# Kernel optimization log

Measured on AMD Instinct MI355X. Metric: run time of the kernel, lower is better.

## Reference

```python
import jax, jax.numpy as jnp
import numpy as np

D_MODEL = 1024
N_HEADS = 16
HEAD_DIM = D_MODEL // N_HEADS


def setup_inputs() -> dict:
    key = jax.random.key(0)
    ks = jax.random.split(key, 7)
    scale = 1.0 / np.sqrt(D_MODEL)
    x = jax.random.normal(ks[0], (4, 2048, D_MODEL), dtype=jnp.float32)
    Wq = jax.random.normal(ks[1], (D_MODEL, D_MODEL), dtype=jnp.float32) * scale
    Wk = jax.random.normal(ks[2], (D_MODEL, D_MODEL), dtype=jnp.float32) * scale
    Wv = jax.random.normal(ks[3], (D_MODEL, D_MODEL), dtype=jnp.float32) * scale
    bq = jax.random.normal(ks[4], (D_MODEL,), dtype=jnp.float32) * scale
    bk = jax.random.normal(ks[5], (D_MODEL,), dtype=jnp.float32) * scale
    bv = jax.random.normal(ks[6], (D_MODEL,), dtype=jnp.float32) * scale
    return {"x": x, "Wq": Wq, "bq": bq, "Wk": Wk, "bk": bk, "Wv": Wv, "bv": bv}


def reference(x, Wq, bq, Wk, bk, Wv, bv):
    B, S, _ = x.shape
    # Linear projections (torch Linear: x @ W.T + b; W here stored as [in, out])
    q = x @ Wq + bq
    k = x @ Wk + bk
    v = x @ Wv + bv
    # [B, H, S, Dh]
    q = q.reshape(B, S, N_HEADS, HEAD_DIM).transpose(0, 2, 1, 3)
    k = k.reshape(B, S, N_HEADS, HEAD_DIM).transpose(0, 2, 1, 3)
    v = v.reshape(B, S, N_HEADS, HEAD_DIM).transpose(0, 2, 1, 3)
    scores = jnp.einsum("bhqd,bhkd->bhqk", q, k) / jnp.sqrt(jnp.float32(HEAD_DIM))
    probs = jax.nn.softmax(scores, axis=-1)
    out = jnp.einsum("bhqk,bhkd->bhqd", probs, v)
    return out.transpose(0, 2, 1, 3).reshape(B, S, D_MODEL)
```

## Files before the change

### kernel.cpp

```cpp
#include <hip/hip_runtime.h>
#include <math.h>

#define DM   1024
#define SEQ  2048
#define BAT  4
#define NH   16
#define DH   64
#define MTOT (BAT*SEQ)
#define NKT  (SEQ/64)

typedef __attribute__((ext_vector_type(8))) short bf16x8;
typedef __attribute__((ext_vector_type(4))) short bf16x4;
typedef __attribute__((ext_vector_type(4))) float f32x4;
typedef __attribute__((ext_vector_type(16))) float f32x16;
typedef __attribute__((ext_vector_type(4))) unsigned int u32x4;

static __device__ __forceinline__ unsigned short f2bf(float f) {
    union { float f; unsigned u; } x; x.f = f;
    unsigned r = x.u + 0x7fffu + ((x.u >> 16) & 1u);
    return (unsigned short)(r >> 16);
}

static __device__ __forceinline__ void load_lds16(const void* g, void* l) {
    __builtin_amdgcn_global_load_lds(
        (const __attribute__((address_space(1))) unsigned int*)g,
        (__attribute__((address_space(3))) unsigned int*)l,
        16, 0, 0);
}

__global__ __launch_bounds__(256)
void xcvt(const float* __restrict__ x, unsigned short* __restrict__ out, int n8)
{
    for (int i = blockIdx.x * blockDim.x + threadIdx.x; i < n8; i += gridDim.x * blockDim.x) {
        float4 a = reinterpret_cast<const float4*>(x)[2 * i];
        float4 b = reinterpret_cast<const float4*>(x)[2 * i + 1];
        ushort4 lo, hi;
        lo.x = f2bf(a.x); lo.y = f2bf(a.y); lo.z = f2bf(a.z); lo.w = f2bf(a.w);
        hi.x = f2bf(b.x); hi.y = f2bf(b.y); hi.z = f2bf(b.z); hi.w = f2bf(b.w);
        reinterpret_cast<ushort4*>(out)[2 * i]     = lo;
        reinterpret_cast<ushort4*>(out)[2 * i + 1] = hi;
    }
}

__global__ __launch_bounds__(256)
void wtcvt(const float* __restrict__ Wq, const float* __restrict__ Wk,
           const float* __restrict__ Wv, unsigned short* __restrict__ Wt)
{
    const float* W = (blockIdx.z == 0) ? Wq : (blockIdx.z == 1) ? Wk : Wv;
    unsigned short* out = Wt + (size_t)blockIdx.z * DM * DM;

    __shared__ float Ts[64][65];
    const int t  = threadIdx.x;
    const int k0 = blockIdx.y * 64;
    const int n0 = blockIdx.x * 64;

    const int r  = t >> 4;
    const int c4 = (t & 15) * 4;
#pragma unroll
    for (int u = 0; u < 4; ++u) {
        float4 v = *reinterpret_cast<const float4*>(&W[(size_t)(k0 + r + u * 16) * DM + n0 + c4]);
        Ts[r + u * 16][c4 + 0] = v.x;
        Ts[r + u * 16][c4 + 1] = v.y;
        Ts[r + u * 16][c4 + 2] = v.z;
        Ts[r + u * 16][c4 + 3] = v.w;
    }
    __syncthreads();

    const int n   = t >> 2;
    const int kk0 = (t & 3) * 16;
#pragma unroll
    for (int j = 0; j < 4; ++j) {
        ushort4 o;
        o.x = f2bf(Ts[kk0 + j * 4 + 0][n]);
        o.y = f2bf(Ts[kk0 + j * 4 + 1][n]);
        o.z = f2bf(Ts[kk0 + j * 4 + 2][n]);
        o.w = f2bf(Ts[kk0 + j * 4 + 3][n]);
        *reinterpret_cast<ushort4*>(&out[(size_t)(n0 + n) * DM + k0 + kk0 + j * 4]) = o;
    }
}

#define GBM 128
#define GBN 128
#define GBK 64
#define GNT (DM/GBK)

__global__ __launch_bounds__(256)
void qkv_mfma(const unsigned short* __restrict__ Xb,
              const unsigned short* __restrict__ Wt,
              const float* __restrict__ bq, const float* __restrict__ bk,
              const float* __restrict__ bv,
              unsigned short* __restrict__ Qw, unsigned short* __restrict__ Kw,
              unsigned short* __restrict__ Vt)
{
    __shared__ __align__(16) unsigned short As[2][GBM][GBK];
    __shared__ __align__(16) unsigned short Bs[2][GBN][GBK];

    const int t    = threadIdx.x;
    const int lane = t & 63;
    const int w    = t >> 6;
    const int g    = lane >> 4;
    const int c    = lane & 15;
    const int wm   = w >> 1;
    const int wn   = w & 1;

    const int cpx = gridDim.x >> 3;
    const int swz = (blockIdx.x & 7) * cpx + (blockIdx.x >> 3);
    const int tn  = swz % (3072 / GBN);
    const int tm  = swz / (3072 / GBN);
    const int m0  = tm * GBM;
    const int n0  = tn * GBN;

    const int srow  = lane >> 3;
    const int sswz  = ((lane & 7) * 16) ^ (16 * (srow & 7));
    const int rbase = w * 32;

#define GSTAGE(buf, kt)                                                               \
    do {                                                                              \
        const size_t kb = (size_t)(kt) * GBK;                                         \
        _Pragma("unroll")                                                             \
        for (int u = 0; u < 4; ++u) {                                                 \
            const int row = rbase + u * 8;                                            \
            load_lds16((const char*)(Xb + (size_t)(m0 + row + srow) * DM + kb) + sswz,\
                       (void*)&As[buf][row][0]);                                      \
        }                                                                             \
        _Pragma("unroll")                                                             \
        for (int u = 0; u < 4; ++u) {                                                 \
            const int row = rbase + u * 8;                                            \
            load_lds16((const char*)(Wt + (size_t)(n0 + row + srow) * DM + kb) + sswz,\
                       (void*)&Bs[buf][row][0]);                                      \
        }                                                                             \
    } while (0)

    f32x4 acc[4][4];
#pragma unroll
    for (int i = 0; i < 4; ++i)
#pragma unroll
        for (int j = 0; j < 4; ++j) { acc[i][j][0] = 0.f; acc[i][j][1] = 0.f; acc[i][j][2] = 0.f; acc[i][j][3] = 0.f; }

    GSTAGE(0, 0);

    for (int kt = 0; kt < GNT; ++kt) {
        const int cb = kt & 1;
        if (kt + 1 < GNT) GSTAGE(cb ^ 1, kt + 1);
        __syncthreads();

#pragma unroll
        for (int ks = 0; ks < 2; ++ks) {
            bf16x8 af[4], bf[4];
#pragma unroll
            for (int mb = 0; mb < 4; ++mb) {
                const int row = wm * 64 + mb * 16 + c;
                const int off = (ks * 64 + g * 16) ^ (16 * (row & 7));
                af[mb] = *reinterpret_cast<const bf16x8*>((const char*)&As[cb][row][0] + off);
            }
#pragma unroll
            for (int nb = 0; nb < 4; ++nb) {
                const int row = wn * 64 + nb * 16 + c;
                const int off = (ks * 64 + g * 16) ^ (16 * (row & 7));
                bf[nb] = *reinterpret_cast<const bf16x8*>((const char*)&Bs[cb][row][0] + off);
            }
#pragma unroll
            for (int mb = 0; mb < 4; ++mb)
#pragma unroll
                for (int nb = 0; nb < 4; ++nb)
                    acc[mb][nb] = __builtin_amdgcn_mfma_f32_16x16x32_bf16(af[mb], bf[nb], acc[mb][nb], 0, 0, 0);
        }

        __syncthreads();
    }

    const int p   = n0 >> 10;
    const int nl0 = (n0 & 1023) + wn * 64;
    const float* bias = (p == 0) ? bq : (p == 1) ? bk : bv;

#pragma unroll
    for (int nb = 0; nb < 4; ++nb) {
        const int col = nl0 + nb * 16 + c;
        const float bv_ = bias[col];
#pragma unroll
        for (int mb = 0; mb < 4; ++mb) {
            const int mrow0 = m0 + wm * 64 + mb * 16 + 4 * g;
            if (p == 0) {
#pragma unroll
                for (int i = 0; i < 4; ++i)
                    Qw[(size_t)(mrow0 + i) * DM + col] = f2bf((acc[mb][nb][i] + bv_) * 0.125f);
            } else if (p == 1) {
#pragma unroll
                for (int i = 0; i < 4; ++i)
                    Kw[(size_t)(mrow0 + i) * DM + col] = f2bf(acc[mb][nb][i] + bv_);
            } else {
                const int hh = col >> 6, dd = col & 63;
                const int bb = mrow0 >> 11, ss = mrow0 & (SEQ - 1);
                ushort4 o;
                o.x = f2bf(acc[mb][nb][0] + bv_);
                o.y = f2bf(acc[mb][nb][1] + bv_);
                o.z = f2bf(acc[mb][nb][2] + bv_);
                o.w = f2bf(acc[mb][nb][3] + bv_);
                *reinterpret_cast<ushort4*>(&Vt[((size_t)(bb * NH + hh) * DH + dd) * SEQ + ss]) = o;
            }
        }
    }
#undef GSTAGE
}

__global__ __launch_bounds__(256, 3)
void attn_mfma32(const unsigned short* __restrict__ Qw,
                 const unsigned short* __restrict__ Kw,
                 const unsigned short* __restrict__ Vt,
                 float* __restrict__ O)
{
    __shared__ __align__(16) unsigned short Kt[2][64][64];
    __shared__ __align__(16) unsigned short Vs[2][64][64];
    __shared__ float Lbuf[4][32];

    const int t    = threadIdx.x;
    const int lane = t & 63;
    const int w    = t >> 6;
    const int q    = lane & 31;
    const int hi   = lane >> 5;

    const int q0 = blockIdx.x * 128;
    const int h  = blockIdx.y;
    const int b  = blockIdx.z;

    const size_t kqbase = ((size_t)b * SEQ) * DM + (size_t)h * DH;
    const size_t vbase  = ((size_t)(b * NH + h) * DH) * SEQ;

    bf16x8 qf[4];
    {
        const unsigned short* qrow = Qw + kqbase + (size_t)(q0 + 32 * w + q) * DM;
#pragma unroll
        for (int ks = 0; ks < 4; ++ks)
            qf[ks] = *reinterpret_cast<const bf16x8*>(qrow + 16 * ks + 8 * hi);
    }

    f32x16 oacc[2];
#pragma unroll
    for (int dt = 0; dt < 2; ++dt)
#pragma unroll
        for (int i = 0; i < 16; ++i) oacc[dt][i] = 0.f;
    float lpart = 0.f;

    const int srow = lane >> 3;
    const int sswz = ((lane & 7) * 16) ^ (16 * (srow & 7));
    const int r0   = w * 16;

#define STAGE_TILE(buf, kt)                                                          \
    do {                                                                             \
        _Pragma("unroll")                                                            \
        for (int u = 0; u < 2; ++u) {                                                \
            const int key = (kt) * 64 + r0 + u * 8 + srow;                           \
            load_lds16((const char*)(Kw + kqbase + (size_t)key * DM) + sswz,         \
                       (void*)&Kt[buf][r0 + u * 8][0]);                              \
        }                                                                            \
        _Pragma("unroll")                                                            \
        for (int u = 0; u < 2; ++u) {                                                \
            const int d = r0 + u * 8 + srow;                                         \
            load_lds16((const char*)(Vt + vbase + (size_t)d * SEQ + (kt) * 64) + sswz,\
                       (void*)&Vs[buf][r0 + u * 8][0]);                              \
        }                                                                            \
    } while (0)

    STAGE_TILE(0, 0);

    const int swzb = 16 * (lane & 7);

    for (int kt = 0; kt < NKT; ++kt) {
        const int cb = kt & 1;
        if (kt + 1 < NKT) STAGE_TILE(cb ^ 1, kt + 1);
        __syncthreads();

        f32x16 st[2];
#pragma unroll
        for (int kt2 = 0; kt2 < 2; ++kt2) {
            f32x16 z;
#pragma unroll
            for (int i = 0; i < 16; ++i) z[i] = 0.f;
#pragma unroll
            for (int ks = 0; ks < 4; ++ks) {
                const int off = (32 * ks + 16 * hi) ^ swzb;
                bf16x8 kf = *reinterpret_cast<const bf16x8*>(
                    (const char*)&Kt[cb][kt2 * 32 + q][0] + off);
                z = __builtin_amdgcn_mfma_f32_32x32x16_bf16(kf, qf[ks], z, 0, 0, 0);
            }
            st[kt2] = z;
        }

        unsigned Dw[2][8];
#pragma unroll
        for (int kt2 = 0; kt2 < 2; ++kt2)
#pragma unroll
            for (int j = 0; j < 8; ++j) {
                const float e0 = __expf(st[kt2][2 * j]);
                const float e1 = __expf(st[kt2][2 * j + 1]);
                lpart += e0 + e1;
                unsigned d;
                asm("v_cvt_pk_bf16_f32 %0, %1, %2" : "=v"(d) : "v"(e0), "v"(e1));
                Dw[kt2][j] = d;
            }

        bf16x8 pf[4];
#pragma unroll
        for (int ks = 0; ks < 4; ++ks) {
            const int kt2 = ks >> 1, lw = ks & 1;
            unsigned a0 = Dw[kt2][4 * lw + 0];
            unsigned a1 = Dw[kt2][4 * lw + 1];
            unsigned a2 = Dw[kt2][4 * lw + 2];
            unsigned a3 = Dw[kt2][4 * lw + 3];
            asm volatile("v_permlane32_swap_b32 %0, %1" : "+v"(a0), "+v"(a2));
            asm volatile("v_permlane32_swap_b32 %0, %1" : "+v"(a1), "+v"(a3));
            u32x4 tv; tv[0] = a0; tv[1] = a1; tv[2] = a2; tv[3] = a3;
            pf[ks] = __builtin_bit_cast(bf16x8, tv);
        }

#pragma unroll
        for (int dt = 0; dt < 2; ++dt)
#pragma unroll
            for (int ks = 0; ks < 4; ++ks) {
                const int off = (32 * ks + 16 * hi) ^ swzb;
                bf16x8 vf = *reinterpret_cast<const bf16x8*>(
                    (const char*)&Vs[cb][dt * 32 + q][0] + off);
                oacc[dt] = __builtin_amdgcn_mfma_f32_32x32x16_bf16(pf[ks], vf, oacc[dt], 0, 0, 0);
            }

        __syncthreads();
    }

    const float ltot = lpart + __shfl_xor(lpart, 32);
    const float inv  = 1.0f / ltot;
    if (lane < 32) Lbuf[w][q] = inv;

    float* obase = O + ((size_t)(b * SEQ + q0 + 32 * w)) * DM + h * DH;
#pragma unroll
    for (int j = 0; j < 4; ++j) {
        f32x4 iv = *reinterpret_cast<const f32x4*>(&Lbuf[w][8 * j + 4 * hi]);
#pragma unroll
        for (int i = 0; i < 4; ++i) {
            const int r   = 4 * j + i;
            const int row = 8 * j + 4 * hi + i;
#pragma unroll
            for (int dt = 0; dt < 2; ++dt)
                obase[(size_t)row * DM + dt * 32 + q] = oacc[dt][r] * iv[i];
        }
    }
#undef STAGE_TILE
}

extern "C" void kernel_launch(void* const* d_in, const int* in_sizes, int n_in,
                              void* d_out, int out_size, void* d_ws, size_t ws_size,
                              hipStream_t stream) {
    const float* x  = (const float*)d_in[0];
    const float* Wq = (const float*)d_in[1];
    const float* bq = (const float*)d_in[2];
    const float* Wk = (const float*)d_in[3];
    const float* bk = (const float*)d_in[4];
    const float* Wv = (const float*)d_in[5];
    const float* bv = (const float*)d_in[6];
    float* out = (float*)d_out;

    unsigned short* q  = (unsigned short*)d_ws;
    unsigned short* k  = q  + (size_t)MTOT * DM;
    unsigned short* vt = k  + (size_t)MTOT * DM;
    unsigned short* xb = vt + (size_t)MTOT * DM;
    unsigned short* wt = xb + (size_t)MTOT * DM;

    xcvt<<<2048, 256, 0, stream>>>(x, xb, MTOT * DM / 8);
    wtcvt<<<dim3(16, 16, 3), 256, 0, stream>>>(Wq, Wk, Wv, wt);

    qkv_mfma<<<1536, 256, 0, stream>>>(xb, wt, bq, bk, bv, q, k, vt);

    dim3 g2(SEQ / 128, NH, BAT);
    attn_mfma32<<<g2, dim3(256), 0, stream>>>(q, k, vt, out);
}
```

Before: 177.3 us.

## Double query rows per attention block, use exp2 with folded log2e scale

Each wave now handles 64 query rows (two 32-row sub-blocks), so every K/V tile in LDS is reused by twice as many MFMAs. The grid shrinks to 512 blocks with a swizzled block-to-(batch, head, q-tile) mapping. The softmax scale now folds log2(e) into Q so the kernel can call the hardware exp2 directly. Barriers are replaced with explicit waitcnt plus s_barrier so the next tile's prefetch stays in flight. The cost is higher register pressure (launch bounds drop to 2 blocks per SM) and fewer blocks, which may lower occupancy and load balance.

```diff
diff --git a/kernel.cpp b/kernel.cpp
--- a/kernel.cpp
+++ b/kernel.cpp
@@ -15,10 +15,16 @@
 typedef __attribute__((ext_vector_type(16))) float f32x16;
 typedef __attribute__((ext_vector_type(4))) unsigned int u32x4;
 
+#define QSCALE 0.18033688011112042f
+
 static __device__ __forceinline__ unsigned short f2bf(float f) {
     union { float f; unsigned u; } x; x.f = f;
     unsigned r = x.u + 0x7fffu + ((x.u >> 16) & 1u);
     return (unsigned short)(r >> 16);
+}
+
+static __device__ __forceinline__ float hexp2(float x) {
+    return __builtin_amdgcn_exp2f(x);
 }
 
 static __device__ __forceinline__ void load_lds16(const void* g, void* l) {
@@ -183,7 +189,7 @@
             if (p == 0) {
 #pragma unroll
                 for (int i = 0; i < 4; ++i)
-                    Qw[(size_t)(mrow0 + i) * DM + col] = f2bf((acc[mb][nb][i] + bv_) * 0.125f);
+                    Qw[(size_t)(mrow0 + i) * DM + col] = f2bf((acc[mb][nb][i] + bv_) * QSCALE);
             } else if (p == 1) {
 #pragma unroll
                 for (int i = 0; i < 4; ++i)
@@ -203,15 +209,15 @@
 #undef GSTAGE
 }
 
-__global__ __launch_bounds__(256, 3)
-void attn_mfma32(const unsigned short* __restrict__ Qw,
+__global__ __launch_bounds__(256, 2)
+void attn_mfma64(const unsigned short* __restrict__ Qw,
                  const unsigned short* __restrict__ Kw,
                  const unsigned short* __restrict__ Vt,
                  float* __restrict__ O)
 {
     __shared__ __align__(16) unsigned short Kt[2][64][64];
     __shared__ __align__(16) unsigned short Vs[2][64][64];
-    __shared__ float Lbuf[4][32];
+    __shared__ float Lbuf[4][2][32];
 
     const int t    = threadIdx.x;
     const int lane = t & 63;
@@ -219,27 +225,33 @@
     const int q    = lane & 31;
     const int hi   = lane >> 5;
 
-    const int q0 = blockIdx.x * 128;
-    const int h  = blockIdx.y;
-    const int b  = blockIdx.z;
+    const int bid = blockIdx.x;
+    const int ii  = bid >> 3;
+    const int hd  = (bid & 7) * 8 + (ii >> 3);
+    const int b   = hd >> 4;
+    const int h   = hd & 15;
+    const int q0  = (ii & 7) * 256;
 
     const size_t kqbase = ((size_t)b * SEQ) * DM + (size_t)h * DH;
     const size_t vbase  = ((size_t)(b * NH + h) * DH) * SEQ;
 
-    bf16x8 qf[4];
-    {
-        const unsigned short* qrow = Qw + kqbase + (size_t)(q0 + 32 * w + q) * DM;
+    bf16x8 qf[2][4];
+#pragma unroll
+    for (int qb = 0; qb < 2; ++qb) {
+        const unsigned short* qrow = Qw + kqbase + (size_t)(q0 + 64 * w + 32 * qb + q) * DM;
 #pragma unroll
         for (int ks = 0; ks < 4; ++ks)
-            qf[ks] = *reinterpret_cast<const bf16x8*>(qrow + 16 * ks + 8 * hi);
-    }
-
-    f32x16 oacc[2];
-#pragma unroll
-    for (int dt = 0; dt < 2; ++dt)
-#pragma unroll
-        for (int i = 0; i < 16; ++i) oacc[dt][i] = 0.f;
-    float lpart = 0.f;
+            qf[qb][ks] = *reinterpret_cast<const bf16x8*>(qrow + 16 * ks + 8 * hi);
+    }
+
+    f32x16 oacc[2][2];
+#pragma unroll
+    for (int qb = 0; qb < 2; ++qb)
+#pragma unroll
+        for (int dt = 0; dt < 2; ++dt)
+#pragma unroll
+            for (int i = 0; i < 16; ++i) oacc[qb][dt][i] = 0.f;
+    float lpart[2] = {0.f, 0.f};
 
     const int srow = lane >> 3;
     const int sswz = ((lane & 7) * 16) ^ (16 * (srow & 7));
@@ -267,50 +279,65 @@
 
     for (int kt = 0; kt < NKT; ++kt) {
         const int cb = kt & 1;
-        if (kt + 1 < NKT) STAGE_TILE(cb ^ 1, kt + 1);
-        __syncthreads();
-
-        f32x16 st[2];
-#pragma unroll
-        for (int kt2 = 0; kt2 < 2; ++kt2) {
-            f32x16 z;
-#pragma unroll
-            for (int i = 0; i < 16; ++i) z[i] = 0.f;
+        if (kt + 1 < NKT) {
+            STAGE_TILE(cb ^ 1, kt + 1);
+            asm volatile("s_waitcnt vmcnt(4)" ::: "memory");
+        } else {
+            asm volatile("s_waitcnt vmcnt(0)" ::: "memory");
+        }
+        __builtin_amdgcn_s_barrier();
+        __builtin_amdgcn_sched_barrier(0);
+
+        bf16x8 kf[2][4];
+#pragma unroll
+        for (int kt2 = 0; kt2 < 2; ++kt2)
 #pragma unroll
             for (int ks = 0; ks < 4; ++ks) {
                 const int off = (32 * ks + 16 * hi) ^ swzb;
-                bf16x8 kf = *reinterpret_cast<const bf16x8*>(
+                kf[kt2][ks] = *reinterpret_cast<const bf16x8*>(
                     (const char*)&Kt[cb][kt2 * 32 + q][0] + off);
-                z = __builtin_amdgcn_mfma_f32_32x32x16_bf16(kf, qf[ks], z, 0, 0, 0);
-            }
-            st[kt2] = z;
-        }
-
-        unsigned Dw[2][8];
-#pragma unroll
-        for (int kt2 = 0; kt2 < 2; ++kt2)
-#pragma unroll
-            for (int j = 0; j < 8; ++j) {
-                const float e0 = __expf(st[kt2][2 * j]);
-                const float e1 = __expf(st[kt2][2 * j + 1]);
-                lpart += e0 + e1;
-                unsigned d;
-                asm("v_cvt_pk_bf16_f32 %0, %1, %2" : "=v"(d) : "v"(e0), "v"(e1));
-                Dw[kt2][j] = d;
-            }
-
-        bf16x8 pf[4];
-#pragma unroll
-        for (int ks = 0; ks < 4; ++ks) {
-            const int kt2 = ks >> 1, lw = ks & 1;
-            unsigned a0 = Dw[kt2][4 * lw + 0];
-            unsigned a1 = Dw[kt2][4 * lw + 1];
-            unsigned a2 = Dw[kt2][4 * lw + 2];
-            unsigned a3 = Dw[kt2][4 * lw + 3];
-            asm volatile("v_permlane32_swap_b32 %0, %1" : "+v"(a0), "+v"(a2));
-            asm volatile("v_permlane32_swap_b32 %0, %1" : "+v"(a1), "+v"(a3));
-            u32x4 tv; tv[0] = a0; tv[1] = a1; tv[2] = a2; tv[3] = a3;
-            pf[ks] = __builtin_bit_cast(bf16x8, tv);
+            }
+
+        bf16x8 pf[2][4];
+#pragma unroll
+        for (int qb = 0; qb < 2; ++qb) {
+            f32x16 st[2];
+#pragma unroll
+            for (int kt2 = 0; kt2 < 2; ++kt2) {
+                f32x16 z;
+#pragma unroll
+                for (int i = 0; i < 16; ++i) z[i] = 0.f;
+#pragma unroll
+                for (int ks = 0; ks < 4; ++ks)
+                    z = __builtin_amdgcn_mfma_f32_32x32x16_bf16(kf[kt2][ks], qf[qb][ks], z, 0, 0, 0);
+                st[kt2] = z;
+            }
+
+            unsigned Dw[2][8];
+#pragma unroll
+            for (int kt2 = 0; kt2 < 2; ++kt2)
+#pragma unroll
+                for (int j = 0; j < 8; ++j) {
+                    const float e0 = hexp2(st[kt2][2 * j]);
+                    const float e1 = hexp2(st[kt2][2 * j + 1]);
+                    lpart[qb] += e0 + e1;
+                    unsigned d;
+                    asm("v_cvt_pk_bf16_f32 %0, %1, %2" : "=v"(d) : "v"(e0), "v"(e1));
+                    Dw[kt2][j] = d;
+                }
+
+#pragma unroll
+            for (int ks = 0; ks < 4; ++ks) {
+                const int kt2 = ks >> 1, lw = ks & 1;
+                unsigned a0 = Dw[kt2][4 * lw + 0];
+                unsigned a1 = Dw[kt2][4 * lw + 1];
+                unsigned a2 = Dw[kt2][4 * lw + 2];
+                unsigned a3 = Dw[kt2][4 * lw + 3];
+                asm volatile("v_permlane32_swap_b32 %0, %1" : "+v"(a0), "+v"(a2));
+                asm volatile("v_permlane32_swap_b32 %0, %1" : "+v"(a1), "+v"(a3));
+                u32x4 tv; tv[0] = a0; tv[1] = a1; tv[2] = a2; tv[3] = a3;
+                pf[qb][ks] = __builtin_bit_cast(bf16x8, tv);
+            }
         }
 
 #pragma unroll
@@ -320,27 +347,36 @@
                 const int off = (32 * ks + 16 * hi) ^ swzb;
                 bf16x8 vf = *reinterpret_cast<const bf16x8*>(
                     (const char*)&Vs[cb][dt * 32 + q][0] + off);
-                oacc[dt] = __builtin_amdgcn_mfma_f32_32x32x16_bf16(pf[ks], vf, oacc[dt], 0, 0, 0);
-            }
-
-        __syncthreads();
-    }
-
-    const float ltot = lpart + __shfl_xor(lpart, 32);
-    const float inv  = 1.0f / ltot;
-    if (lane < 32) Lbuf[w][q] = inv;
-
-    float* obase = O + ((size_t)(b * SEQ + q0 + 32 * w)) * DM + h * DH;
-#pragma unroll
-    for (int j = 0; j < 4; ++j) {
-        f32x4 iv = *reinterpret_cast<const f32x4*>(&Lbuf[w][8 * j + 4 * hi]);
-#pragma unroll
-        for (int i = 0; i < 4; ++i) {
-            const int r   = 4 * j + i;
-            const int row = 8 * j + 4 * hi + i;
-#pragma unroll
-            for (int dt = 0; dt < 2; ++dt)
-                obase[(size_t)row * DM + dt * 32 + q] = oacc[dt][r] * iv[i];
+                oacc[0][dt] = __builtin_amdgcn_mfma_f32_32x32x16_bf16(pf[0][ks], vf, oacc[0][dt], 0, 0, 0);
+                oacc[1][dt] = __builtin_amdgcn_mfma_f32_32x32x16_bf16(pf[1][ks], vf, oacc[1][dt], 0, 0, 0);
+            }
+
+        asm volatile("s_waitcnt lgkmcnt(0)" ::: "memory");
+        __builtin_amdgcn_s_barrier();
+        __builtin_amdgcn_sched_barrier(0);
+    }
+
+#pragma unroll
+    for (int qb = 0; qb < 2; ++qb) {
+        const float ltot = lpart[qb] + __shfl_xor(lpart[qb], 32);
+        const float inv  = 1.0f / ltot;
+        if (lane < 32) Lbuf[w][qb][q] = inv;
+    }
+
+#pragma unroll
+    for (int qb = 0; qb < 2; ++qb) {
+        float* obase = O + ((size_t)(b * SEQ + q0 + 64 * w + 32 * qb)) * DM + h * DH;
+#pragma unroll
+        for (int j = 0; j < 4; ++j) {
+            f32x4 iv = *reinterpret_cast<const f32x4*>(&Lbuf[w][qb][8 * j + 4 * hi]);
+#pragma unroll
+            for (int i = 0; i < 4; ++i) {
+                const int r   = 4 * j + i;
+                const int row = 8 * j + 4 * hi + i;
+#pragma unroll
+                for (int dt = 0; dt < 2; ++dt)
+                    obase[(size_t)row * DM + dt * 32 + q] = oacc[qb][dt][r] * iv[i];
+            }
         }
     }
 #undef STAGE_TILE
@@ -369,6 +405,5 @@
 
     qkv_mfma<<<1536, 256, 0, stream>>>(xb, wt, bq, bk, bv, q, k, vt);
 
-    dim3 g2(SEQ / 128, NH, BAT);
-    attn_mfma32<<<g2, dim3(256), 0, stream>>>(q, k, vt, out);
-}
+    attn_mfma64<<<512, 256, 0, stream>>>(q, k, vt, out);
+}
```

New measurement: 164.1 us. 1.08x faster.
